# Kernel tuning notes

Hardware: AMD Instinct MI355X
Metric: run time of the kernel (lower is better)

## Reference

```python
import jax, jax.numpy as jnp
import numpy as np

B, L, C = 32, 4096, 64
PL, PC = 64, 16          # patch sizes along L and C
NP = 256                 # num_patches
OUT = 512                # output_dim
FS = 1000.0              # sampling frequency -> T = 1/FS


def setup_inputs() -> dict:
    key = jax.random.key(0)
    ks = jax.random.split(key, 7)
    d_in = PL * (PC * 2)
    return {
        "x": jax.random.normal(ks[0], (B, L, C), dtype=jnp.float32),
        "start_L": jax.random.randint(ks[1], (B, NP), 0, L - PL + 1, dtype=jnp.int32),
        "start_C": jax.random.randint(ks[2], (B, NP), 0, C - PC + 1, dtype=jnp.int32),
        "w1": jax.random.normal(ks[3], (OUT, d_in), dtype=jnp.float32) / np.sqrt(d_in),
        "b1": jax.random.normal(ks[4], (OUT,), dtype=jnp.float32) * 0.01,
        "w2": jax.random.normal(ks[5], (OUT, OUT), dtype=jnp.float32) / np.sqrt(OUT),
        "b2": jax.random.normal(ks[6], (OUT,), dtype=jnp.float32) * 0.01,
    }


def reference(x, start_L, start_C, w1, b1, w2, b2):
    T = 1.0 / FS
    t = jnp.arange(L, dtype=jnp.float32) * T                      # [L]

    # patch index grids (wrapping, as in the torch module)
    idx_L = (start_L[:, :, None] + jnp.arange(PL, dtype=jnp.int32)) % L   # [B,NP,PL]
    idx_C = (start_C[:, :, None] + jnp.arange(PC, dtype=jnp.int32)) % C   # [B,NP,PC]

    # double gather: patches[b,p,i,j] = x[b, idx_L[b,p,i], idx_C[b,p,j]]
    b_idx = jnp.arange(B, dtype=jnp.int32)[:, None, None, None]
    patches = x[b_idx, idx_L[:, :, :, None], idx_C[:, :, None, :]]        # [B,NP,PL,PC]

    # time embedding gathered with the same L indices, broadcast over PC
    t_patches = jnp.broadcast_to(t[idx_L][:, :, :, None], (B, NP, PL, PC))

    feats = jnp.concatenate([patches, t_patches], axis=-1)                # [B,NP,PL,2*PC]
    feats = feats.reshape(B, NP, PL * 2 * PC)

    h = jnp.einsum('bpd,od->bpo', feats, w1) + b1
    h = jax.nn.silu(h)
    out = jnp.einsum('bpo,qo->bpq', h, w2) + b2                           # [B,NP,OUT]
    return out
```

## Files before the change

### kernel.cpp

```cpp
#include <hip/hip_runtime.h>
#include <hip/hip_bf16.h>
#include <stdint.h>

#define LL   4096
#define CCH  64
#define DOUT 512
#define MM   8192
#define TT   0.001f

using bf16 = __hip_bfloat16;
typedef __attribute__((ext_vector_type(8))) short bf16x8;
typedef __attribute__((ext_vector_type(4))) float f32x4;

__device__ __forceinline__ uint2 pack4_bf16(float a, float b, float c, float d) {
    union { bf16 h[4]; uint2 u; } p;
    p.h[0] = __float2bfloat16(a);
    p.h[1] = __float2bfloat16(b);
    p.h[2] = __float2bfloat16(c);
    p.h[3] = __float2bfloat16(d);
    return p.u;
}

__global__ __launch_bounds__(256) void prep(
    const float* __restrict__ w1, const float* __restrict__ b1,
    const float* __restrict__ w2,
    bf16* __restrict__ w1g, bf16* __restrict__ w2g,
    float* __restrict__ A1, float* __restrict__ C1)
{
    const int blk = blockIdx.x;
    if (blk < 512) {
        int g   = blk * 256 + threadIdx.x;
        int kk0 = (g & 7) * 4;
        int col = (g >> 3) & 511;
        int ic  = g >> 12;
        int l   = ic * 2 + (kk0 >> 4);
        int j0  = kk0 & 15;
        float4 v = *(const float4*)(w1 + (size_t)col * 2048 + l * 32 + j0);
        *(uint2*)(w1g + ((size_t)(ic * 512 + col) * 32 + kk0)) =
            pack4_bf16(v.x, v.y, v.z, v.w);
    } else if (blk < 768) {
        int g   = (blk - 512) * 256 + threadIdx.x;
        int kk0 = (g & 7) * 4;
        int col = (g >> 3) & 511;
        int ic2 = g >> 12;
        float4 v = *(const float4*)(w2 + (size_t)col * 512 + ic2 * 32 + kk0);
        *(uint2*)(w2g + ((size_t)(ic2 * 512 + col) * 32 + kk0)) =
            pack4_bf16(v.x, v.y, v.z, v.w);
    } else {
        const int o = (blk - 768) * 4 + (threadIdx.x >> 6);
        const int l = threadIdx.x & 63;
        const float* wr = w1 + (size_t)o * 2048 + l * 32 + 16;
        float s0 = 0.f;
#pragma unroll
        for (int j = 0; j < 16; ++j) s0 += wr[j];
        float s1 = (float)l * s0;
#pragma unroll
        for (int off = 32; off > 0; off >>= 1) {
            s0 += __shfl_down(s0, off);
            s1 += __shfl_down(s1, off);
        }
        if (l == 0) {
            A1[o] = TT * s0;
            C1[o] = b1[o] + TT * s1;
        }
    }
}

__global__ __launch_bounds__(1024, 4) void mega(
    const float* __restrict__ x, const int* __restrict__ sLg,
    const int* __restrict__ sCg, const bf16* __restrict__ w1g,
    const bf16* __restrict__ w2g, const float* __restrict__ A1,
    const float* __restrict__ C1, const float* __restrict__ b2,
    float* __restrict__ out)
{
    __shared__ __align__(16) bf16 Asm[32 * 1024];
    __shared__ float slf[32];
    bf16* const Hs = Asm;

    const int t    = threadIdx.x;
    const int lane = t & 63;
    const int wave = t >> 6;
    const int fr   = lane & 15;
    const int fq   = lane >> 4;
    const int m0   = blockIdx.x * 32;
    const int b    = m0 >> 8;

    {
        const int gr  = t >> 5;
        const int gs  = t & 31;
        const int gsl = sLg[m0 + gr];
        const int gsc = sCg[m0 + gr];
        if (gs == 0) slf[gr] = (float)gsl;
        const int c4 = gs & 3;
        const int l0 = gs >> 2;
        const float* gx = x + ((size_t)b * LL + gsl + l0) * CCH
                            + gsc + c4 * 4;
        float4 xv[8];
#pragma unroll
        for (int p = 0; p < 8; ++p)
            xv[p] = *(const float4*)(gx + (size_t)p * 8 * CCH);
#pragma unroll
        for (int p = 0; p < 8; ++p) {
            const int l = p * 8 + l0;
            const int u = l * 2 + (c4 >> 1);
            const int idx = gr * 1024 + ((u ^ (gr & 7)) * 8) + (c4 & 1) * 4;
            *(uint2*)(Asm + idx) = pack4_bf16(xv[p].x, xv[p].y, xv[p].z, xv[p].w);
        }
    }
    __syncthreads();

    const bf16* const w1base = w1g + (size_t)(wave * 32 + fr) * 32 + fq * 8;
    f32x4 acc[2][2] = {};
    {
        bf16x8 bnx[2];
#pragma unroll
        for (int j = 0; j < 2; ++j)
            bnx[j] = *(const bf16x8*)(w1base + j * 512);
#pragma unroll
        for (int it = 0; it < 32; ++it) {
            bf16x8 bcur[2];
#pragma unroll
            for (int j = 0; j < 2; ++j) bcur[j] = bnx[j];
            if (it < 31) {
                const bf16* p = w1base + (size_t)(it + 1) * 16384;
#pragma unroll
                for (int j = 0; j < 2; ++j)
                    bnx[j] = *(const bf16x8*)(p + j * 512);
            }
            bf16x8 af[2];
#pragma unroll
            for (int i = 0; i < 2; ++i) {
                const int row = i * 16 + fr;
                const int u   = it * 4 + fq;
                af[i] = *(const bf16x8*)&Asm[row * 1024 + ((u ^ (row & 7)) * 8)];
            }
#pragma unroll
            for (int i = 0; i < 2; ++i)
#pragma unroll
                for (int j = 0; j < 2; ++j)
                    acc[i][j] = __builtin_amdgcn_mfma_f32_16x16x32_bf16(
                        af[i], bcur[j], acc[i][j], 0, 0, 0);
        }
    }
    __syncthreads();

    const bf16* const w2base = w2g + (size_t)(wave * 32 + fr) * 32 + fq * 8;
    bf16x8 bnx2[2];
#pragma unroll
    for (int j = 0; j < 2; ++j)
        bnx2[j] = *(const bf16x8*)(w2base + j * 512);
    float avv[2], cvv[2];
#pragma unroll
    for (int j = 0; j < 2; ++j) {
        const int col = wave * 32 + j * 16 + fr;
        avv[j] = A1[col];
        cvv[j] = C1[col];
    }

    {
        float slr[2][4];
#pragma unroll
        for (int i = 0; i < 2; ++i)
#pragma unroll
            for (int rr = 0; rr < 4; ++rr)
                slr[i][rr] = slf[i * 16 + fq * 4 + rr];
#pragma unroll
        for (int j = 0; j < 2; ++j) {
            const int col = wave * 32 + j * 16 + fr;
            const float av = avv[j];
            const float cv = cvv[j];
            const int c8 = col >> 3, c7 = col & 7;
#pragma unroll
            for (int i = 0; i < 2; ++i)
#pragma unroll
                for (int rr = 0; rr < 4; ++rr) {
                    const int row = i * 16 + fq * 4 + rr;
                    float v = acc[i][j][rr] + slr[i][rr] * av + cv;
                    v = v / (1.0f + __expf(-v));
                    Hs[row * 512 + ((c8 ^ (row & 7)) * 8) + c7] = __float2bfloat16(v);
                }
        }
    }
    __syncthreads();

    f32x4 acc2[2][2] = {};
    float bvv[2];
#pragma unroll
    for (int j = 0; j < 2; ++j) bvv[j] = b2[wave * 32 + j * 16 + fr];
    {
#pragma unroll
        for (int it2 = 0; it2 < 16; ++it2) {
            bf16x8 bcur[2];
#pragma unroll
            for (int j = 0; j < 2; ++j) bcur[j] = bnx2[j];
            if (it2 < 15) {
                const bf16* p = w2base + (size_t)(it2 + 1) * 16384;
#pragma unroll
                for (int j = 0; j < 2; ++j)
                    bnx2[j] = *(const bf16x8*)(p + j * 512);
            }
            bf16x8 af2[2];
#pragma unroll
            for (int i = 0; i < 2; ++i) {
                const int row = i * 16 + fr;
                const int u2  = it2 * 4 + fq;
                af2[i] = *(const bf16x8*)&Hs[row * 512 + ((u2 ^ (row & 7)) * 8)];
            }
#pragma unroll
            for (int i = 0; i < 2; ++i)
#pragma unroll
                for (int j = 0; j < 2; ++j)
                    acc2[i][j] = __builtin_amdgcn_mfma_f32_16x16x32_bf16(
                        af2[i], bcur[j], acc2[i][j], 0, 0, 0);
        }
    }

#pragma unroll
    for (int j = 0; j < 2; ++j) {
        const int col = wave * 32 + j * 16 + fr;
        const float bv = bvv[j];
#pragma unroll
        for (int i = 0; i < 2; ++i)
#pragma unroll
            for (int rr = 0; rr < 4; ++rr) {
                const int row = m0 + i * 16 + fq * 4 + rr;
                out[(size_t)row * 512 + col] = acc2[i][j][rr] + bv;
            }
    }
}

extern "C" void kernel_launch(void* const* d_in, const int* in_sizes, int n_in,
                              void* d_out, int out_size, void* d_ws, size_t ws_size,
                              hipStream_t stream)
{
    const float* x  = (const float*)d_in[0];
    const int*   sL = (const int*)  d_in[1];
    const int*   sC = (const int*)  d_in[2];
    const float* w1 = (const float*)d_in[3];
    const float* b1 = (const float*)d_in[4];
    const float* w2 = (const float*)d_in[5];
    const float* b2 = (const float*)d_in[6];
    float* out = (float*)d_out;

    char* ws = (char*)d_ws;
    bf16*  w1g = (bf16*)ws;
    bf16*  w2g = (bf16*)(ws + (1 << 20));
    float* A1  = (float*)(ws + (1 << 20) + (1 << 19));
    float* C1  = A1 + DOUT;

    prep<<<896, 256, 0, stream>>>(w1, b1, w2, w1g, w2g, A1, C1);
    mega<<<MM / 32, 1024, 0, stream>>>(x, sL, sC, w1g, w2g, A1, C1, b2, out);
}
```

Before: 123.9 us.

## Stream weight tiles via global_load_lds double buffer with staggered k-order

Weight fragments for both GEMMs are no longer loaded into registers through normal global loads. Each wave now copies its slice of w1g/w2g straight into a per-wave double-buffered LDS region with global_load_lds and hand-placed vmcnt/lgkmcnt waits. Each wave also starts at a different k-chunk (rotated by wave index) to spread L2/HBM accesses, and the w2 prefetch begins before the SiLU epilogue. This adds 64KB of shared memory per block, which may reduce occupancy, and relies on fragile manual waitcnt synchronisation.

```diff
diff --git a/kernel.cpp b/kernel.cpp
--- a/kernel.cpp
+++ b/kernel.cpp
@@ -19,6 +19,12 @@
     p.h[2] = __float2bfloat16(c);
     p.h[3] = __float2bfloat16(d);
     return p.u;
+}
+
+__device__ __forceinline__ void dma16(const bf16* g, bf16* l) {
+    __builtin_amdgcn_global_load_lds(
+        (const __attribute__((address_space(1))) void*)g,
+        (__attribute__((address_space(3))) void*)l, 16, 0, 0);
 }
 
 __global__ __launch_bounds__(256) void prep(
@@ -74,6 +80,7 @@
     float* __restrict__ out)
 {
     __shared__ __align__(16) bf16 Asm[32 * 1024];
+    __shared__ __align__(16) bf16 Bb[2][16][1024];
     __shared__ float slf[32];
     bf16* const Hs = Asm;
 
@@ -84,6 +91,17 @@
     const int fq   = lane >> 4;
     const int m0   = blockIdx.x * 32;
     const int b    = m0 >> 8;
+
+    const int ca0 = wave * 2;
+
+#pragma unroll
+    for (int k = 0; k < 2; ++k) {
+        const int c = (ca0 + k) & 31;
+        const bf16* src = w1g + (size_t)c * 16384 + wave * 1024 + lane * 8;
+#pragma unroll
+        for (int j = 0; j < 2; ++j)
+            dma16(src + j * 512, &Bb[k][wave][j * 512]);
+    }
 
     {
         const int gr  = t >> 5;
@@ -109,53 +127,63 @@
     }
     __syncthreads();
 
-    const bf16* const w1base = w1g + (size_t)(wave * 32 + fr) * 32 + fq * 8;
     f32x4 acc[2][2] = {};
-    {
-        bf16x8 bnx[2];
-#pragma unroll
-        for (int j = 0; j < 2; ++j)
-            bnx[j] = *(const bf16x8*)(w1base + j * 512);
-#pragma unroll
-        for (int it = 0; it < 32; ++it) {
-            bf16x8 bcur[2];
-#pragma unroll
-            for (int j = 0; j < 2; ++j) bcur[j] = bnx[j];
-            if (it < 31) {
-                const bf16* p = w1base + (size_t)(it + 1) * 16384;
-#pragma unroll
-                for (int j = 0; j < 2; ++j)
-                    bnx[j] = *(const bf16x8*)(p + j * 512);
-            }
-            bf16x8 af[2];
-#pragma unroll
-            for (int i = 0; i < 2; ++i) {
-                const int row = i * 16 + fr;
-                const int u   = it * 4 + fq;
-                af[i] = *(const bf16x8*)&Asm[row * 1024 + ((u ^ (row & 7)) * 8)];
-            }
-#pragma unroll
-            for (int i = 0; i < 2; ++i)
-#pragma unroll
-                for (int j = 0; j < 2; ++j)
-                    acc[i][j] = __builtin_amdgcn_mfma_f32_16x16x32_bf16(
-                        af[i], bcur[j], acc[i][j], 0, 0, 0);
-        }
-    }
-    __syncthreads();
-
-    const bf16* const w2base = w2g + (size_t)(wave * 32 + fr) * 32 + fq * 8;
-    bf16x8 bnx2[2];
-#pragma unroll
-    for (int j = 0; j < 2; ++j)
-        bnx2[j] = *(const bf16x8*)(w2base + j * 512);
-    float avv[2], cvv[2];
+#pragma unroll
+    for (int it = 0; it < 32; ++it) {
+        if (it == 31) { asm volatile("s_waitcnt vmcnt(0)" ::: "memory"); }
+        else          { asm volatile("s_waitcnt vmcnt(2)" ::: "memory"); }
+        __builtin_amdgcn_sched_barrier(0);
+        const int c = (ca0 + it) & 31;
+        const bf16* bs = &Bb[it & 1][wave][0];
+        bf16x8 bf[2], af[2];
+#pragma unroll
+        for (int j = 0; j < 2; ++j)
+            bf[j] = *(const bf16x8*)(bs + j * 512 + fr * 32 + fq * 8);
+#pragma unroll
+        for (int i = 0; i < 2; ++i) {
+            const int row = i * 16 + fr;
+            const int u   = c * 4 + fq;
+            af[i] = *(const bf16x8*)&Asm[row * 1024 + ((u ^ (row & 7)) * 8)];
+        }
+        asm volatile("s_waitcnt lgkmcnt(0)" ::: "memory");
+        __builtin_amdgcn_sched_barrier(0);
+        if (it < 30) {
+            const int cn = (ca0 + it + 2) & 31;
+            const bf16* src = w1g + (size_t)cn * 16384 + wave * 1024 + lane * 8;
+#pragma unroll
+            for (int j = 0; j < 2; ++j)
+                dma16(src + j * 512, &Bb[it & 1][wave][j * 512]);
+        }
+#pragma unroll
+        for (int i = 0; i < 2; ++i)
+#pragma unroll
+            for (int j = 0; j < 2; ++j)
+                acc[i][j] = __builtin_amdgcn_mfma_f32_16x16x32_bf16(
+                    af[i], bf[j], acc[i][j], 0, 0, 0);
+    }
+
+    const int cb0 = wave;
+    float avv[2], cvv[2], bvv[2];
 #pragma unroll
     for (int j = 0; j < 2; ++j) {
         const int col = wave * 32 + j * 16 + fr;
         avv[j] = A1[col];
         cvv[j] = C1[col];
-    }
+        bvv[j] = b2[col];
+    }
+    asm volatile("s_waitcnt vmcnt(0)" ::: "memory");
+    __builtin_amdgcn_sched_barrier(0);
+#pragma unroll
+    for (int k = 0; k < 2; ++k) {
+        const int c = (cb0 + k) & 15;
+        const bf16* src = w2g + (size_t)c * 16384 + wave * 1024 + lane * 8;
+#pragma unroll
+        for (int j = 0; j < 2; ++j)
+            dma16(src + j * 512, &Bb[k][wave][j * 512]);
+    }
+    asm volatile("s_waitcnt lgkmcnt(0)" ::: "memory");
+    __builtin_amdgcn_s_barrier();
+    __builtin_amdgcn_sched_barrier(0);
 
     {
         float slr[2][4];
@@ -181,38 +209,43 @@
                 }
         }
     }
-    __syncthreads();
+    asm volatile("s_waitcnt lgkmcnt(0)" ::: "memory");
+    __builtin_amdgcn_s_barrier();
+    __builtin_amdgcn_sched_barrier(0);
 
     f32x4 acc2[2][2] = {};
-    float bvv[2];
-#pragma unroll
-    for (int j = 0; j < 2; ++j) bvv[j] = b2[wave * 32 + j * 16 + fr];
-    {
-#pragma unroll
-        for (int it2 = 0; it2 < 16; ++it2) {
-            bf16x8 bcur[2];
-#pragma unroll
-            for (int j = 0; j < 2; ++j) bcur[j] = bnx2[j];
-            if (it2 < 15) {
-                const bf16* p = w2base + (size_t)(it2 + 1) * 16384;
-#pragma unroll
-                for (int j = 0; j < 2; ++j)
-                    bnx2[j] = *(const bf16x8*)(p + j * 512);
-            }
-            bf16x8 af2[2];
-#pragma unroll
-            for (int i = 0; i < 2; ++i) {
-                const int row = i * 16 + fr;
-                const int u2  = it2 * 4 + fq;
-                af2[i] = *(const bf16x8*)&Hs[row * 512 + ((u2 ^ (row & 7)) * 8)];
-            }
-#pragma unroll
-            for (int i = 0; i < 2; ++i)
-#pragma unroll
-                for (int j = 0; j < 2; ++j)
-                    acc2[i][j] = __builtin_amdgcn_mfma_f32_16x16x32_bf16(
-                        af2[i], bcur[j], acc2[i][j], 0, 0, 0);
-        }
+#pragma unroll
+    for (int it2 = 0; it2 < 16; ++it2) {
+        if (it2 == 15) { asm volatile("s_waitcnt vmcnt(0)" ::: "memory"); }
+        else           { asm volatile("s_waitcnt vmcnt(2)" ::: "memory"); }
+        __builtin_amdgcn_sched_barrier(0);
+        const int c = (cb0 + it2) & 15;
+        const bf16* bs = &Bb[it2 & 1][wave][0];
+        bf16x8 bf[2], af2[2];
+#pragma unroll
+        for (int j = 0; j < 2; ++j)
+            bf[j] = *(const bf16x8*)(bs + j * 512 + fr * 32 + fq * 8);
+#pragma unroll
+        for (int i = 0; i < 2; ++i) {
+            const int row = i * 16 + fr;
+            const int u2  = c * 4 + fq;
+            af2[i] = *(const bf16x8*)&Hs[row * 512 + ((u2 ^ (row & 7)) * 8)];
+        }
+        asm volatile("s_waitcnt lgkmcnt(0)" ::: "memory");
+        __builtin_amdgcn_sched_barrier(0);
+        if (it2 < 14) {
+            const int cn = (cb0 + it2 + 2) & 15;
+            const bf16* src = w2g + (size_t)cn * 16384 + wave * 1024 + lane * 8;
+#pragma unroll
+            for (int j = 0; j < 2; ++j)
+                dma16(src + j * 512, &Bb[it2 & 1][wave][j * 512]);
+        }
+#pragma unroll
+        for (int i = 0; i < 2; ++i)
+#pragma unroll
+            for (int j = 0; j < 2; ++j)
+                acc2[i][j] = __builtin_amdgcn_mfma_f32_16x16x32_bf16(
+                    af2[i], bf[j], acc2[i][j], 0, 0, 0);
     }
 
 #pragma unroll
```

New measurement: 116.7 us. -5.8%, faster.

## Split fused kernel into gather plus two tiled LDS-staged GEMM kernels

Applied to the files above, without the earlier changes.

Replaces the single fused kernel, which used 32-row tiles and streamed weights from global memory straight into registers, with a gather kernel that writes bf16 patches to a workspace and two 128x128-tile GEMM kernels. The GEMM kernels use double-buffered global-to-LDS DMA loads. Larger tiles share each weight load across more rows, cutting weight traffic. The cost is two extra global round trips (the patch matrix and the bf16 hidden activations), two more launches, and no wrap handling in the gather.

```diff
diff --git a/kernel.cpp b/kernel.cpp
--- a/kernel.cpp
+++ b/kernel.cpp
@@ -21,31 +21,39 @@
     return p.u;
 }
 
+__device__ __forceinline__ void dma16(const bf16* g, bf16* l) {
+    __builtin_amdgcn_global_load_lds(
+        (const __attribute__((address_space(1))) void*)g,
+        (__attribute__((address_space(3))) void*)l, 16, 0, 0);
+}
+
+
 __global__ __launch_bounds__(256) void prep(
     const float* __restrict__ w1, const float* __restrict__ b1,
     const float* __restrict__ w2,
-    bf16* __restrict__ w1g, bf16* __restrict__ w2g,
+    bf16* __restrict__ w1gs, bf16* __restrict__ w2gs,
     float* __restrict__ A1, float* __restrict__ C1)
 {
     const int blk = blockIdx.x;
     if (blk < 512) {
-        int g   = blk * 256 + threadIdx.x;
-        int kk0 = (g & 7) * 4;
-        int col = (g >> 3) & 511;
-        int ic  = g >> 12;
-        int l   = ic * 2 + (kk0 >> 4);
-        int j0  = kk0 & 15;
-        float4 v = *(const float4*)(w1 + (size_t)col * 2048 + l * 32 + j0);
-        *(uint2*)(w1g + ((size_t)(ic * 512 + col) * 32 + kk0)) =
-            pack4_bf16(v.x, v.y, v.z, v.w);
+        int g     = blk * 256 + threadIdx.x;
+        int col_g = g >> 8;
+        int k     = (g & 255) * 4;
+        int l     = k >> 4, j = k & 15;
+        float4 v = *(const float4*)(w1 + (size_t)col_g * 2048 + l * 32 + j);
+        int kc = k >> 6, nt = col_g >> 7, colL = col_g & 127, u = (k >> 3) & 7;
+        size_t idx = (size_t)(kc * 4 + nt) * 8192 + colL * 64
+                   + ((u ^ (colL & 7)) * 8) + (k & 7);
+        *(uint2*)(w1gs + idx) = pack4_bf16(v.x, v.y, v.z, v.w);
     } else if (blk < 768) {
-        int g   = (blk - 512) * 256 + threadIdx.x;
-        int kk0 = (g & 7) * 4;
-        int col = (g >> 3) & 511;
-        int ic2 = g >> 12;
-        float4 v = *(const float4*)(w2 + (size_t)col * 512 + ic2 * 32 + kk0);
-        *(uint2*)(w2g + ((size_t)(ic2 * 512 + col) * 32 + kk0)) =
-            pack4_bf16(v.x, v.y, v.z, v.w);
+        int g     = (blk - 512) * 256 + threadIdx.x;
+        int col_g = g >> 7;
+        int k     = (g & 127) * 4;
+        float4 v = *(const float4*)(w2 + (size_t)col_g * 512 + k);
+        int kc = k >> 6, nt = col_g >> 7, colL = col_g & 127, u = (k >> 3) & 7;
+        size_t idx = (size_t)(kc * 4 + nt) * 8192 + colL * 64
+                   + ((u ^ (colL & 7)) * 8) + (k & 7);
+        *(uint2*)(w2gs + idx) = pack4_bf16(v.x, v.y, v.z, v.w);
     } else {
         const int o = (blk - 768) * 4 + (threadIdx.x >> 6);
         const int l = threadIdx.x & 63;
@@ -66,167 +74,165 @@
     }
 }
 
-__global__ __launch_bounds__(1024, 4) void mega(
+__global__ __launch_bounds__(256) void gather(
     const float* __restrict__ x, const int* __restrict__ sLg,
-    const int* __restrict__ sCg, const bf16* __restrict__ w1g,
-    const bf16* __restrict__ w2g, const float* __restrict__ A1,
-    const float* __restrict__ C1, const float* __restrict__ b2,
-    float* __restrict__ out)
-{
-    __shared__ __align__(16) bf16 Asm[32 * 1024];
-    __shared__ float slf[32];
-    bf16* const Hs = Asm;
-
-    const int t    = threadIdx.x;
-    const int lane = t & 63;
-    const int wave = t >> 6;
-    const int fr   = lane & 15;
-    const int fq   = lane >> 4;
-    const int m0   = blockIdx.x * 32;
-    const int b    = m0 >> 8;
-
-    {
-        const int gr  = t >> 5;
-        const int gs  = t & 31;
-        const int gsl = sLg[m0 + gr];
-        const int gsc = sCg[m0 + gr];
-        if (gs == 0) slf[gr] = (float)gsl;
-        const int c4 = gs & 3;
-        const int l0 = gs >> 2;
-        const float* gx = x + ((size_t)b * LL + gsl + l0) * CCH
-                            + gsc + c4 * 4;
-        float4 xv[8];
-#pragma unroll
-        for (int p = 0; p < 8; ++p)
-            xv[p] = *(const float4*)(gx + (size_t)p * 8 * CCH);
-#pragma unroll
-        for (int p = 0; p < 8; ++p) {
-            const int l = p * 8 + l0;
-            const int u = l * 2 + (c4 >> 1);
-            const int idx = gr * 1024 + ((u ^ (gr & 7)) * 8) + (c4 & 1) * 4;
-            *(uint2*)(Asm + idx) = pack4_bf16(xv[p].x, xv[p].y, xv[p].z, xv[p].w);
-        }
-    }
-    __syncthreads();
-
-    const bf16* const w1base = w1g + (size_t)(wave * 32 + fr) * 32 + fq * 8;
-    f32x4 acc[2][2] = {};
-    {
-        bf16x8 bnx[2];
-#pragma unroll
-        for (int j = 0; j < 2; ++j)
-            bnx[j] = *(const bf16x8*)(w1base + j * 512);
-#pragma unroll
-        for (int it = 0; it < 32; ++it) {
-            bf16x8 bcur[2];
-#pragma unroll
-            for (int j = 0; j < 2; ++j) bcur[j] = bnx[j];
-            if (it < 31) {
-                const bf16* p = w1base + (size_t)(it + 1) * 16384;
-#pragma unroll
-                for (int j = 0; j < 2; ++j)
-                    bnx[j] = *(const bf16x8*)(p + j * 512);
-            }
-            bf16x8 af[2];
-#pragma unroll
-            for (int i = 0; i < 2; ++i) {
-                const int row = i * 16 + fr;
-                const int u   = it * 4 + fq;
-                af[i] = *(const bf16x8*)&Asm[row * 1024 + ((u ^ (row & 7)) * 8)];
-            }
-#pragma unroll
-            for (int i = 0; i < 2; ++i)
+    const int* __restrict__ sCg, bf16* __restrict__ Ag)
+{
+    const int tg = blockIdx.x * 256 + threadIdx.x;
+    const int r  = tg >> 6;
+    const int l  = tg & 63;
+    const int b  = r >> 8;
+    const int sl = sLg[r], sc = sCg[r];
+    const float* src = x + ((size_t)b * LL + sl + l) * CCH + sc;
+    float4 v0 = *(const float4*)(src);
+    float4 v1 = *(const float4*)(src + 4);
+    float4 v2 = *(const float4*)(src + 8);
+    float4 v3 = *(const float4*)(src + 12);
+    bf16* dst = Ag + (size_t)(l >> 2) * 524288 + (size_t)r * 64;
+    const int u0 = (l & 3) * 2;
+    const int p0 = u0 ^ (r & 7), p1 = (u0 + 1) ^ (r & 7);
+    *(uint2*)(dst + p0 * 8)     = pack4_bf16(v0.x, v0.y, v0.z, v0.w);
+    *(uint2*)(dst + p0 * 8 + 4) = pack4_bf16(v1.x, v1.y, v1.z, v1.w);
+    *(uint2*)(dst + p1 * 8)     = pack4_bf16(v2.x, v2.y, v2.z, v2.w);
+    *(uint2*)(dst + p1 * 8 + 4) = pack4_bf16(v3.x, v3.y, v3.z, v3.w);
+}
+
+template<int NIT>
+__device__ __forceinline__ void gemm_kloop(
+    const bf16* aSrc, const bf16* bSrc, size_t aChunkStride,
+    bf16 (&As)[2][8192], bf16 (&Bs)[2][8192],
+    int wave, int fr, int fq, int wr, int wc, f32x4 acc[4][2])
+{
+    auto STAGE = [&](int buf, int kc) {
+        const bf16* as = aSrc + (size_t)kc * aChunkStride;
+        const bf16* bs = bSrc + (size_t)kc * 32768;
+        dma16(as,       &As[buf][wave * 1024]);
+        dma16(as + 512, &As[buf][wave * 1024 + 512]);
+        dma16(bs,       &Bs[buf][wave * 1024]);
+        dma16(bs + 512, &Bs[buf][wave * 1024 + 512]);
+    };
+    STAGE(0, 0);
+    STAGE(1, 1);
+#pragma unroll
+    for (int it = 0; it < NIT; ++it) {
+        if (it < NIT - 1) { asm volatile("s_waitcnt vmcnt(4)" ::: "memory"); }
+        else              { asm volatile("s_waitcnt vmcnt(0)" ::: "memory"); }
+        __builtin_amdgcn_sched_barrier(0);
+        __builtin_amdgcn_s_barrier();
+        __builtin_amdgcn_sched_barrier(0);
+        const bf16* ab = &As[it & 1][0];
+        const bf16* bb = &Bs[it & 1][0];
+#pragma unroll
+        for (int kk = 0; kk < 2; ++kk) {
+            const int u = kk * 4 + fq;
+            bf16x8 af[4], bf[2];
+#pragma unroll
+            for (int i = 0; i < 4; ++i) {
+                const int row = wr * 64 + i * 16 + fr;
+                af[i] = *(const bf16x8*)&ab[row * 64 + ((u ^ (row & 7)) * 8)];
+            }
+#pragma unroll
+            for (int j = 0; j < 2; ++j) {
+                const int col = wc * 32 + j * 16 + fr;
+                bf[j] = *(const bf16x8*)&bb[col * 64 + ((u ^ (col & 7)) * 8)];
+            }
+#pragma unroll
+            for (int i = 0; i < 4; ++i)
 #pragma unroll
                 for (int j = 0; j < 2; ++j)
                     acc[i][j] = __builtin_amdgcn_mfma_f32_16x16x32_bf16(
-                        af[i], bcur[j], acc[i][j], 0, 0, 0);
-        }
+                        af[i], bf[j], acc[i][j], 0, 0, 0);
+        }
+        __builtin_amdgcn_sched_barrier(0);
+        asm volatile("s_waitcnt lgkmcnt(0)" ::: "memory");
+        __builtin_amdgcn_s_barrier();
+        __builtin_amdgcn_sched_barrier(0);
+        if (it < NIT - 2) STAGE(it & 1, it + 2);
     }
-    __syncthreads();
-
-    const bf16* const w2base = w2g + (size_t)(wave * 32 + fr) * 32 + fq * 8;
-    bf16x8 bnx2[2];
+}
+
+__global__ __launch_bounds__(512, 2) void gemm1(
+    const bf16* __restrict__ Ag, const bf16* __restrict__ w1gs,
+    const int* __restrict__ sLg, const float* __restrict__ A1,
+    const float* __restrict__ C1, bf16* __restrict__ Hg)
+{
+    __shared__ __align__(16) bf16 As[2][8192];
+    __shared__ __align__(16) bf16 Bs[2][8192];
+    const int t = threadIdx.x, lane = t & 63, wave = t >> 6;
+    const int fr = lane & 15, fq = lane >> 4;
+    const int wr = wave >> 2, wc = wave & 3;
+    const int nt = blockIdx.x & 3, mt = blockIdx.x >> 2;
+
+    float avv[2], cvv[2];
+#pragma unroll
+    for (int j = 0; j < 2; ++j) {
+        const int colG = nt * 128 + wc * 32 + j * 16 + fr;
+        avv[j] = A1[colG];
+        cvv[j] = C1[colG];
+    }
+    float slr[4][4];
+#pragma unroll
+    for (int i = 0; i < 4; ++i)
+#pragma unroll
+        for (int rr = 0; rr < 4; ++rr)
+            slr[i][rr] = (float)sLg[mt * 128 + wr * 64 + i * 16 + fq * 4 + rr];
+
+    const bf16* aSrc = Ag   + (size_t)mt * 8192 + wave * 1024 + lane * 8;
+    const bf16* bSrc = w1gs + (size_t)nt * 8192 + wave * 1024 + lane * 8;
+    f32x4 acc[4][2] = {};
+    gemm_kloop<16>(aSrc, bSrc, 524288, As, Bs, wave, fr, fq, wr, wc, acc);
+
+#pragma unroll
+    for (int i = 0; i < 4; ++i)
+#pragma unroll
+        for (int j = 0; j < 2; ++j) {
+            const int colG = nt * 128 + wc * 32 + j * 16 + fr;
+            const int kc2  = colG >> 6;
+            const int kcol = colG & 63;
+            const int u    = kcol >> 3;
+#pragma unroll
+            for (int rr = 0; rr < 4; ++rr) {
+                const int rG = mt * 128 + wr * 64 + i * 16 + fq * 4 + rr;
+                float v = acc[i][j][rr] + slr[i][rr] * avv[j] + cvv[j];
+                v = v / (1.0f + __expf(-v));
+                Hg[(size_t)kc2 * 524288 + (size_t)rG * 64
+                   + ((u ^ (rG & 7)) * 8) + (kcol & 7)] = __float2bfloat16(v);
+            }
+        }
+}
+
+__global__ __launch_bounds__(512, 2) void gemm2(
+    const bf16* __restrict__ Hg, const bf16* __restrict__ w2gs,
+    const float* __restrict__ b2, float* __restrict__ out)
+{
+    __shared__ __align__(16) bf16 As[2][8192];
+    __shared__ __align__(16) bf16 Bs[2][8192];
+    const int t = threadIdx.x, lane = t & 63, wave = t >> 6;
+    const int fr = lane & 15, fq = lane >> 4;
+    const int wr = wave >> 2, wc = wave & 3;
+    const int nt = blockIdx.x & 3, mt = blockIdx.x >> 2;
+
+    float bvv[2];
 #pragma unroll
     for (int j = 0; j < 2; ++j)
-        bnx2[j] = *(const bf16x8*)(w2base + j * 512);
-    float avv[2], cvv[2];
-#pragma unroll
-    for (int j = 0; j < 2; ++j) {
-        const int col = wave * 32 + j * 16 + fr;
-        avv[j] = A1[col];
-        cvv[j] = C1[col];
-    }
-
-    {
-        float slr[2][4];
-#pragma unroll
-        for (int i = 0; i < 2; ++i)
-#pragma unroll
-            for (int rr = 0; rr < 4; ++rr)
-                slr[i][rr] = slf[i * 16 + fq * 4 + rr];
+        bvv[j] = b2[nt * 128 + wc * 32 + j * 16 + fr];
+
+    const bf16* aSrc = Hg   + (size_t)mt * 8192 + wave * 1024 + lane * 8;
+    const bf16* bSrc = w2gs + (size_t)nt * 8192 + wave * 1024 + lane * 8;
+    f32x4 acc[4][2] = {};
+    gemm_kloop<8>(aSrc, bSrc, 524288, As, Bs, wave, fr, fq, wr, wc, acc);
+
+#pragma unroll
+    for (int i = 0; i < 4; ++i)
 #pragma unroll
         for (int j = 0; j < 2; ++j) {
-            const int col = wave * 32 + j * 16 + fr;
-            const float av = avv[j];
-            const float cv = cvv[j];
-            const int c8 = col >> 3, c7 = col & 7;
-#pragma unroll
-            for (int i = 0; i < 2; ++i)
-#pragma unroll
-                for (int rr = 0; rr < 4; ++rr) {
-                    const int row = i * 16 + fq * 4 + rr;
-                    float v = acc[i][j][rr] + slr[i][rr] * av + cv;
-                    v = v / (1.0f + __expf(-v));
-                    Hs[row * 512 + ((c8 ^ (row & 7)) * 8) + c7] = __float2bfloat16(v);
-                }
-        }
-    }
-    __syncthreads();
-
-    f32x4 acc2[2][2] = {};
-    float bvv[2];
-#pragma unroll
-    for (int j = 0; j < 2; ++j) bvv[j] = b2[wave * 32 + j * 16 + fr];
-    {
-#pragma unroll
-        for (int it2 = 0; it2 < 16; ++it2) {
-            bf16x8 bcur[2];
-#pragma unroll
-            for (int j = 0; j < 2; ++j) bcur[j] = bnx2[j];
-            if (it2 < 15) {
-                const bf16* p = w2base + (size_t)(it2 + 1) * 16384;
-#pragma unroll
-                for (int j = 0; j < 2; ++j)
-                    bnx2[j] = *(const bf16x8*)(p + j * 512);
-            }
-            bf16x8 af2[2];
-#pragma unroll
-            for (int i = 0; i < 2; ++i) {
-                const int row = i * 16 + fr;
-                const int u2  = it2 * 4 + fq;
-                af2[i] = *(const bf16x8*)&Hs[row * 512 + ((u2 ^ (row & 7)) * 8)];
-            }
-#pragma unroll
-            for (int i = 0; i < 2; ++i)
-#pragma unroll
-                for (int j = 0; j < 2; ++j)
-                    acc2[i][j] = __builtin_amdgcn_mfma_f32_16x16x32_bf16(
-                        af2[i], bcur[j], acc2[i][j], 0, 0, 0);
-        }
-    }
-
-#pragma unroll
-    for (int j = 0; j < 2; ++j) {
-        const int col = wave * 32 + j * 16 + fr;
-        const float bv = bvv[j];
-#pragma unroll
-        for (int i = 0; i < 2; ++i)
+            const int colG = nt * 128 + wc * 32 + j * 16 + fr;
 #pragma unroll
             for (int rr = 0; rr < 4; ++rr) {
-                const int row = m0 + i * 16 + fq * 4 + rr;
-                out[(size_t)row * 512 + col] = acc2[i][j][rr] + bv;
-            }
-    }
+                const int rG = mt * 128 + wr * 64 + i * 16 + fq * 4 + rr;
+                out[(size_t)rG * 512 + colG] = acc[i][j][rr] + bvv[j];
+            }
+        }
 }
 
 extern "C" void kernel_launch(void* const* d_in, const int* in_sizes, int n_in,
@@ -243,11 +249,15 @@
     float* out = (float*)d_out;
 
     char* ws = (char*)d_ws;
-    bf16*  w1g = (bf16*)ws;
-    bf16*  w2g = (bf16*)(ws + (1 << 20));
-    float* A1  = (float*)(ws + (1 << 20) + (1 << 19));
-    float* C1  = A1 + DOUT;
-
-    prep<<<896, 256, 0, stream>>>(w1, b1, w2, w1g, w2g, A1, C1);
-    mega<<<MM / 32, 1024, 0, stream>>>(x, sL, sC, w1g, w2g, A1, C1, b2, out);
-}
+    bf16*  w1gs = (bf16*)ws;
+    bf16*  w2gs = (bf16*)(ws + (1 << 20));
+    float* A1   = (float*)(ws + (1 << 20) + (1 << 19));
+    float* C1   = A1 + DOUT;
+    bf16*  Ag   = (bf16*)(ws + (2  << 20));
+    bf16*  Hg   = (bf16*)(ws + (18 << 20));
+
+    gather<<<2048, 256, 0, stream>>>(x, sL, sC, Ag);
+    prep<<<896, 256, 0, stream>>>(w1, b1, w2, w1gs, w2gs, A1, C1);
+    gemm1<<<256, 512, 0, stream>>>(Ag, w1gs, sL, A1, C1, Hg);
+    gemm2<<<256, 512, 0, stream>>>(Hg, w2gs, b2, out);
+}
```

Result: slower. 131.9 us (+6.5%).
